# Kernel optimization log

Hardware: AMD Instinct MI355X
Metric: run time of the kernel (lower is better)

## Reference

```python
import jax, jax.numpy as jnp
import numpy as np

N_NODES = 20000
STEPS = 10  # message_passing_steps


def _mlp(x, p):
    # 3-layer MLP: Linear->ReLU->Linear->ReLU->Linear (no final activation)
    W1, b1, W2, b2, W3, b3 = p
    h = jax.nn.relu(x @ W1 + b1)
    h = jax.nn.relu(h @ W2 + b2)
    return h @ W3 + b3


def _aggregate(dst, edge_attr, num_nodes):
    # scatter_add of edge features into destination nodes, degree-normalized (deg clamped to >=1)
    agg = jax.ops.segment_sum(edge_attr, dst, num_segments=num_nodes)
    deg = jax.ops.segment_sum(jnp.ones((dst.shape[0], 1), edge_attr.dtype), dst, num_segments=num_nodes)
    return agg / jnp.maximum(deg, 1.0)


def setup_inputs() -> dict:
    key = jax.random.key(0)
    N, EM, EC = N_NODES, 120000, 20000
    ND, MD, CD, OD, L = 12, 7, 4, 3, 128
    keys = iter(jax.random.split(key, 128))

    def lin(i, o):
        return (jax.random.normal(next(keys), (i, o), jnp.float32) * 0.05,
                jax.random.normal(next(keys), (o,), jnp.float32) * 0.05)

    inp = {
        "node_x": jax.random.normal(next(keys), (N, ND), jnp.float32),
        "mesh_edge_attr": jax.random.normal(next(keys), (EM, MD), jnp.float32),
        "contact_edge_attr": jax.random.normal(next(keys), (EC, CD), jnp.float32),
    }
    dims = {"ne": (ND, L), "me": (MD, L), "ce": (CD, L), "pe": (3 * L, L), "pn": (3 * L, L), "de": (L, OD)}
    for name, (i, o) in dims.items():
        W1, b1 = lin(i, L)
        W2, b2 = lin(L, L)
        W3, b3 = lin(L, o)
        for pn, p in zip(["W1", "b1", "W2", "b2", "W3", "b3"], [W1, b1, W2, b2, W3, b3]):
            inp[name + "_" + pn] = p
    inp["mesh_edge_index"] = jax.random.randint(next(keys), (2, EM), 0, N)
    inp["contact_edge_index"] = jax.random.randint(next(keys), (2, EC), 0, N)
    return inp


def reference(node_x, mesh_edge_attr, contact_edge_attr,
              ne_W1, ne_b1, ne_W2, ne_b2, ne_W3, ne_b3,
              me_W1, me_b1, me_W2, me_b2, me_W3, me_b3,
              ce_W1, ce_b1, ce_W2, ce_b2, ce_W3, ce_b3,
              pe_W1, pe_b1, pe_W2, pe_b2, pe_W3, pe_b3,
              pn_W1, pn_b1, pn_W2, pn_b2, pn_W3, pn_b3,
              de_W1, de_b1, de_W2, de_b2, de_W3, de_b3,
              mesh_edge_index, contact_edge_index):
    ne = (ne_W1, ne_b1, ne_W2, ne_b2, ne_W3, ne_b3)
    mep = (me_W1, me_b1, me_W2, me_b2, me_W3, me_b3)
    cep = (ce_W1, ce_b1, ce_W2, ce_b2, ce_W3, ce_b3)
    pe = (pe_W1, pe_b1, pe_W2, pe_b2, pe_W3, pe_b3)
    pn = (pn_W1, pn_b1, pn_W2, pn_b2, pn_W3, pn_b3)
    de = (de_W1, de_b1, de_W2, de_b2, de_W3, de_b3)
    N = node_x.shape[0]
    # encode
    x = _mlp(node_x, ne)                 # [N, 128]
    me = _mlp(mesh_edge_attr, mep)       # [EM, 128]
    ce = _mlp(contact_edge_attr, cep)    # [EC, 128]
    msrc, mdst = mesh_edge_index[0], mesh_edge_index[1]
    csrc, cdst = contact_edge_index[0], contact_edge_index[1]
    # process (shared edge_mlp for both edge types, residual updates)
    for _ in range(STEPS):
        me = me + _mlp(jnp.concatenate([x[msrc], x[mdst], me], axis=-1), pe)
        ce = ce + _mlp(jnp.concatenate([x[csrc], x[cdst], ce], axis=-1), pe)
        agg_m = _aggregate(mdst, me, N)
        agg_c = _aggregate(cdst, ce, N)
        x = x + _mlp(jnp.concatenate([x, agg_m, agg_c], axis=-1), pn)
    # decode
    return _mlp(x, de)                   # [N, 3]
```

## Files before the change

### kernel.cpp

```cpp
#include <hip/hip_runtime.h>
#include <stdint.h>

typedef unsigned short u16;
typedef __attribute__((ext_vector_type(8))) short bf16x8;
typedef __attribute__((ext_vector_type(4))) float f32x4;

#define NNODES 20000
#define EM 120000
#define EC 20000
#define LDIM 128
#define MT 32
#define A_STR 392
#define H_STR 136

__device__ __forceinline__ u16 f2bf(float f){
  uint32_t b = __float_as_uint(f);
  b += 0x7FFF + ((b >> 16) & 1);
  return (u16)(b >> 16);
}

template<int KB>
__device__ __forceinline__ void layer(const u16* sIn, int in_str, const u16* Wp,
                                      int wr, int wc, int lane, f32x4 acc[4]){
  const int row = wr*16 + (lane & 15);
  const int kg  = lane >> 4;
  #pragma unroll
  for (int kb = 0; kb < KB; ++kb){
    bf16x8 a = *(const bf16x8*)(sIn + row*in_str + kb*32 + kg*8);
    const u16* wb = Wp + (((kb*8 + wc*4)*64 + lane) << 3);
    #pragma unroll
    for (int nf = 0; nf < 4; ++nf){
      bf16x8 b = *(const bf16x8*)(wb + (nf << 9));
      acc[nf] = __builtin_amdgcn_mfma_f32_16x16x32_bf16(a, b, acc[nf], 0, 0, 0);
    }
  }
}

__device__ __forceinline__ void hid_epi(f32x4 acc[4], const float* bias,
                                        int wr, int wc, int lane, u16* sOut){
  const int cl = lane & 15;
  const int r0 = wr*16 + (lane >> 4)*4;
  #pragma unroll
  for (int nf = 0; nf < 4; ++nf){
    int col = wc*64 + nf*16 + cl;
    float bv = bias[col];
    #pragma unroll
    for (int r = 0; r < 4; ++r){
      float v = acc[nf][r] + bv;
      sOut[(r0 + r)*H_STR + col] = f2bf(v > 0.f ? v : 0.f);
    }
  }
}

__device__ __forceinline__ void zero4(f32x4 acc[4]){
  const f32x4 vz = {0.f, 0.f, 0.f, 0.f};
  #pragma unroll
  for (int i = 0; i < 4; ++i) acc[i] = vz;
}

struct PackDesc { const float* src; int K_raw, N_raw, NF, elem_off; };
struct PackArgs { PackDesc d[18]; int total; };

__global__ __launch_bounds__(256) void pack_weights(PackArgs pa, u16* dst){
  int idx = blockIdx.x*256 + threadIdx.x;
  if (idx >= pa.total) return;
  int di = 0;
  #pragma unroll
  for (int i = 1; i < 18; ++i) if (idx >= pa.d[i].elem_off) di = i;
  PackDesc dd = pa.d[di];
  int e = idx - dd.elem_off;
  int f = e >> 9, lane = (e >> 3) & 63, j = e & 7;
  int kb = f / dd.NF, nf = f % dd.NF;
  int k = kb*32 + (lane >> 4)*8 + j;
  int n = nf*16 + (lane & 15);
  float v = (k < dd.K_raw && n < dd.N_raw) ? dd.src[k*dd.N_raw + n] : 0.f;
  dst[idx] = f2bf(v);
}

__global__ __launch_bounds__(256) void hist_kernel(const int* mdst, const int* cdst,
                                                   int* cnt_m, int* cnt_c){
  int i = blockIdx.x*256 + threadIdx.x;
  if (i < EM) atomicAdd(&cnt_m[mdst[i]], 1);
  else if (i < EM + EC) atomicAdd(&cnt_c[cdst[i - EM]], 1);
}

struct ScanArgs { const int *cnt_m, *cnt_c; int *start_m, *start_c, *cur_m, *cur_c; };

__global__ __launch_bounds__(256) void scan_kernel(ScanArgs a){
  const int n = NNODES;
  const int* cnt = blockIdx.x == 0 ? a.cnt_m : a.cnt_c;
  int* start     = blockIdx.x == 0 ? a.start_m : a.start_c;
  int* cur       = blockIdx.x == 0 ? a.cur_m : a.cur_c;
  __shared__ int part[256];
  __shared__ int base[257];
  int t = threadIdx.x;
  const int per = (n + 255) / 256;
  int lo = t*per, hi = min(n, lo + per);
  int s = 0;
  for (int j = lo; j < hi; ++j) s += cnt[j];
  part[t] = s;
  __syncthreads();
  if (t == 0){
    int run = 0;
    for (int i = 0; i < 256; ++i){ base[i] = run; run += part[i]; }
    base[256] = run;
  }
  __syncthreads();
  int run = base[t];
  for (int j = lo; j < hi; ++j){ start[j] = run; cur[j] = run; run += cnt[j]; }
  if (t == 255) start[n] = base[256];
}

__global__ __launch_bounds__(256) void scatter_kernel(const int* mdst, const int* cdst,
                                                      int* cur_m, int* cur_c,
                                                      int* eid_m, int* eid_c){
  int i = blockIdx.x*256 + threadIdx.x;
  if (i < EM){
    int p = atomicAdd(&cur_m[mdst[i]], 1);
    eid_m[p] = i;
  } else if (i < EM + EC){
    int e = i - EM;
    int p = atomicAdd(&cur_c[cdst[e]], 1);
    eid_c[p] = e;
  }
}

struct EncArgs {
  const float* in; int Kraw;
  const u16 *Wp1, *Wp2, *Wp3;
  const float *b1, *b2, *b3;
  float* out_f32; u16* out_b16;
};

__global__ __launch_bounds__(256) void enc_kernel(EncArgs a){
  __shared__ u16 sA[MT*A_STR];
  __shared__ u16 sH[MT*H_STR];
  const int tid = threadIdx.x, lane = tid & 63, w = tid >> 6, wr = w & 1, wc = w >> 1;
  const int m0 = blockIdx.x * MT;
  for (int i = tid; i < MT*32; i += 256){
    int row = i >> 5, c = i & 31;
    float v = (c < a.Kraw) ? a.in[(size_t)(m0 + row)*a.Kraw + c] : 0.f;
    sA[row*A_STR + c] = f2bf(v);
  }
  __syncthreads();
  f32x4 acc[4]; zero4(acc);
  layer<1>(sA, A_STR, a.Wp1, wr, wc, lane, acc);
  hid_epi(acc, a.b1, wr, wc, lane, sH);
  __syncthreads();
  zero4(acc);
  layer<4>(sH, H_STR, a.Wp2, wr, wc, lane, acc);
  hid_epi(acc, a.b2, wr, wc, lane, sA);
  __syncthreads();
  zero4(acc);
  layer<4>(sA, H_STR, a.Wp3, wr, wc, lane, acc);
  const int cl = lane & 15, r0l = wr*16 + (lane >> 4)*4;
  #pragma unroll
  for (int nf = 0; nf < 4; ++nf){
    int col = wc*64 + nf*16 + cl;
    float bv = a.b3[col];
    #pragma unroll
    for (int r = 0; r < 4; ++r){
      int m = m0 + r0l + r;
      float v = acc[nf][r] + bv;
      a.out_f32[(size_t)m*LDIM + col] = v;
      a.out_b16[(size_t)m*LDIM + col] = f2bf(v);
    }
  }
}

struct EdgeArgs {
  const u16 *Wp1, *Wp2, *Wp3;
  const float *b1, *b2, *b3;
  const u16* x_b16;
  const int *msrc, *mdst, *csrc, *cdst;
  u16 *me_b16, *ce_b16;
  float *me_f32, *ce_f32;
  int mesh_blocks;
};

__global__ __launch_bounds__(256) void edge_kernel(EdgeArgs a){
  __shared__ u16 sA[MT*A_STR];
  __shared__ u16 sH[MT*H_STR];
  const int tid = threadIdx.x, lane = tid & 63, w = tid >> 6, wr = w & 1, wc = w >> 1;
  const bool mesh = (int)blockIdx.x < a.mesh_blocks;
  const int e0 = (mesh ? (int)blockIdx.x : (int)blockIdx.x - a.mesh_blocks) * MT;
  const int* src = mesh ? a.msrc : a.csrc;
  const int* dst = mesh ? a.mdst : a.cdst;
  u16* fb   = mesh ? a.me_b16 : a.ce_b16;
  float* ff = mesh ? a.me_f32 : a.ce_f32;

  for (int i = tid; i < MT*48; i += 256){
    int row = i/48, ch = i%48;
    int e = e0 + row;
    const u16* sp;
    if (ch < 16)       sp = a.x_b16 + (size_t)src[e]*LDIM + ch*8;
    else if (ch < 32)  sp = a.x_b16 + (size_t)dst[e]*LDIM + (ch-16)*8;
    else               sp = fb + (size_t)e*LDIM + (ch-32)*8;
    *(bf16x8*)(sA + row*A_STR + ch*8) = *(const bf16x8*)sp;
  }
  __syncthreads();
  f32x4 acc[4]; zero4(acc);
  layer<12>(sA, A_STR, a.Wp1, wr, wc, lane, acc);
  hid_epi(acc, a.b1, wr, wc, lane, sH);
  __syncthreads();
  zero4(acc);
  layer<4>(sH, H_STR, a.Wp2, wr, wc, lane, acc);
  hid_epi(acc, a.b2, wr, wc, lane, sA);
  __syncthreads();
  zero4(acc);
  layer<4>(sA, H_STR, a.Wp3, wr, wc, lane, acc);

  const int cl = lane & 15, r0l = wr*16 + (lane >> 4)*4;
  #pragma unroll
  for (int r = 0; r < 4; ++r){
    int e = e0 + r0l + r;
    #pragma unroll
    for (int nf = 0; nf < 4; ++nf){
      int col = wc*64 + nf*16 + cl;
      float nv = ff[(size_t)e*LDIM + col] + acc[nf][r] + a.b3[col];
      ff[(size_t)e*LDIM + col] = nv;
      fb[(size_t)e*LDIM + col] = f2bf(nv);
    }
  }
}

struct NodeArgs {
  const u16 *Wp1, *Wp2, *Wp3;
  const float *b1, *b2, *b3;
  const u16* x_b16_in;
  const float *me_f32, *ce_f32;
  const int *start_m, *eid_m, *start_c, *eid_c;
  float* x_f32; u16* x_b16_out;
};

__global__ __launch_bounds__(256) void node_kernel(NodeArgs a){
  __shared__ u16 sA[MT*A_STR];
  __shared__ u16 sH[MT*H_STR];
  const int tid = threadIdx.x, lane = tid & 63, w = tid >> 6, wr = w & 1, wc = w >> 1;
  const int n0 = blockIdx.x * MT;

  for (int i = tid; i < MT*16; i += 256){
    int row = i >> 4, ch = i & 15;
    *(bf16x8*)(sA + row*A_STR + ch*8) = *(const bf16x8*)(a.x_b16_in + (size_t)(n0+row)*LDIM + ch*8);
  }

  {
    const int r = tid >> 3, c0 = (tid & 7) * 16;
    const int n = n0 + r;
    {
      int s = a.start_m[n], e = a.start_m[n+1];
      f32x4 a0{0,0,0,0}, a1{0,0,0,0}, a2{0,0,0,0}, a3{0,0,0,0};
      for (int j = s; j < e; ++j){
        const f32x4* p = (const f32x4*)(a.me_f32 + (size_t)a.eid_m[j]*LDIM + c0);
        a0 += p[0]; a1 += p[1]; a2 += p[2]; a3 += p[3];
      }
      float inv = 1.f / fmaxf((float)(e - s), 1.f);
      bf16x8 t0, t1;
      #pragma unroll
      for (int k = 0; k < 4; ++k){
        t0[k]   = (short)f2bf(a0[k]*inv); t0[k+4] = (short)f2bf(a1[k]*inv);
        t1[k]   = (short)f2bf(a2[k]*inv); t1[k+4] = (short)f2bf(a3[k]*inv);
      }
      *(bf16x8*)(sA + r*A_STR + 128 + c0) = t0;
      *(bf16x8*)(sA + r*A_STR + 128 + c0 + 8) = t1;
    }
    {
      int s = a.start_c[n], e = a.start_c[n+1];
      f32x4 a0{0,0,0,0}, a1{0,0,0,0}, a2{0,0,0,0}, a3{0,0,0,0};
      for (int j = s; j < e; ++j){
        const f32x4* p = (const f32x4*)(a.ce_f32 + (size_t)a.eid_c[j]*LDIM + c0);
        a0 += p[0]; a1 += p[1]; a2 += p[2]; a3 += p[3];
      }
      float inv = 1.f / fmaxf((float)(e - s), 1.f);
      bf16x8 t0, t1;
      #pragma unroll
      for (int k = 0; k < 4; ++k){
        t0[k]   = (short)f2bf(a0[k]*inv); t0[k+4] = (short)f2bf(a1[k]*inv);
        t1[k]   = (short)f2bf(a2[k]*inv); t1[k+4] = (short)f2bf(a3[k]*inv);
      }
      *(bf16x8*)(sA + r*A_STR + 256 + c0) = t0;
      *(bf16x8*)(sA + r*A_STR + 256 + c0 + 8) = t1;
    }
  }
  __syncthreads();
  f32x4 acc[4]; zero4(acc);
  layer<12>(sA, A_STR, a.Wp1, wr, wc, lane, acc);
  hid_epi(acc, a.b1, wr, wc, lane, sH);
  __syncthreads();
  zero4(acc);
  layer<4>(sH, H_STR, a.Wp2, wr, wc, lane, acc);
  hid_epi(acc, a.b2, wr, wc, lane, sA);
  __syncthreads();
  zero4(acc);
  layer<4>(sA, H_STR, a.Wp3, wr, wc, lane, acc);

  const int cl = lane & 15, r0l = wr*16 + (lane >> 4)*4;
  #pragma unroll
  for (int r = 0; r < 4; ++r){
    int n = n0 + r0l + r;
    #pragma unroll
    for (int nf = 0; nf < 4; ++nf){
      int col = wc*64 + nf*16 + cl;
      float nv = a.x_f32[(size_t)n*LDIM + col] + acc[nf][r] + a.b3[col];
      a.x_f32[(size_t)n*LDIM + col] = nv;
      a.x_b16_out[(size_t)n*LDIM + col] = f2bf(nv);
    }
  }
}

struct DecArgs {
  const u16 *Wp1, *Wp2, *Wp3;
  const float *b1, *b2, *b3;
  const u16* x_b16; float* out;
};

__global__ __launch_bounds__(256) void dec_kernel(DecArgs a){
  __shared__ u16 sA[MT*A_STR];
  __shared__ u16 sH[MT*H_STR];
  const int tid = threadIdx.x, lane = tid & 63, w = tid >> 6, wr = w & 1, wc = w >> 1;
  const int n0 = blockIdx.x * MT;
  for (int i = tid; i < MT*16; i += 256){
    int row = i >> 4, ch = i & 15;
    *(bf16x8*)(sA + row*H_STR + ch*8) = *(const bf16x8*)(a.x_b16 + (size_t)(n0+row)*LDIM + ch*8);
  }
  __syncthreads();
  f32x4 acc[4]; zero4(acc);
  layer<4>(sA, H_STR, a.Wp1, wr, wc, lane, acc);
  hid_epi(acc, a.b1, wr, wc, lane, sH);
  __syncthreads();
  zero4(acc);
  layer<4>(sH, H_STR, a.Wp2, wr, wc, lane, acc);
  hid_epi(acc, a.b2, wr, wc, lane, sA);
  __syncthreads();
  if (wc == 0){
    f32x4 a3 = {0.f, 0.f, 0.f, 0.f};
    const int row = wr*16 + (lane & 15), kg = lane >> 4;
    #pragma unroll
    for (int kb = 0; kb < 4; ++kb){
      bf16x8 av = *(const bf16x8*)(sA + row*H_STR + kb*32 + kg*8);
      bf16x8 bv = *(const bf16x8*)(a.Wp3 + ((kb*64 + lane) << 3));
      a3 = __builtin_amdgcn_mfma_f32_16x16x32_bf16(av, bv, a3, 0, 0, 0);
    }
    const int cl = lane & 15, r0l = wr*16 + (lane >> 4)*4;
    if (cl < 3){
      #pragma unroll
      for (int r = 0; r < 4; ++r)
        a.out[(size_t)(n0 + r0l + r)*3 + cl] = a3[r] + a.b3[cl];
    }
  }
}

extern "C" void kernel_launch(void* const* d_in, const int* in_sizes, int n_in,
                              void* d_out, int out_size, void* d_ws, size_t ws_size,
                              hipStream_t stream){
  auto F = [&](int i){ return (const float*)d_in[i]; };
  const float* node_x   = F(0);
  const float* mesh_attr = F(1);
  const float* cont_attr = F(2);
  const int* mei = (const int*)d_in[39];
  const int* cei = (const int*)d_in[40];
  const int *msrc = mei, *mdst = mei + EM, *csrc = cei, *cdst = cei + EC;

  char* ws = (char*)d_ws;
  size_t off = 0;
  auto take = [&](size_t b)->void*{ void* p = ws + off; off += (b + 255) & ~(size_t)255; return p; };
  float* x_f32  = (float*)take((size_t)NNODES*LDIM*4);
  u16*   x_b16  = (u16*)  take((size_t)NNODES*LDIM*2);
  float* me_f32 = (float*)take((size_t)EM*LDIM*4);
  u16*   me_b16 = (u16*)  take((size_t)EM*LDIM*2);
  float* ce_f32 = (float*)take((size_t)EC*LDIM*4);
  u16*   ce_b16 = (u16*)  take((size_t)EC*LDIM*2);
  u16*   wpack  = (u16*)  take((size_t)309248*2);
  int* cnt_m   = (int*)take((size_t)NNODES*4);
  int* cnt_c   = (int*)take((size_t)NNODES*4);
  int* start_m = (int*)take((size_t)(NNODES+1)*4);
  int* start_c = (int*)take((size_t)(NNODES+1)*4);
  int* cur_m   = (int*)take((size_t)NNODES*4);
  int* cur_c   = (int*)take((size_t)NNODES*4);
  int* eid_m   = (int*)take((size_t)EM*4);
  int* eid_c   = (int*)take((size_t)EC*4);

  static const int tbl[18][5] = {
    {3,12,128,32,128},{5,128,128,128,128},{7,128,128,128,128},
    {9,7,128,32,128},{11,128,128,128,128},{13,128,128,128,128},
    {15,4,128,32,128},{17,128,128,128,128},{19,128,128,128,128},
    {21,384,128,384,128},{23,128,128,128,128},{25,128,128,128,128},
    {27,384,128,384,128},{29,128,128,128,128},{31,128,128,128,128},
    {33,128,128,128,128},{35,128,128,128,128},{37,128,3,128,16}};
  PackArgs pa; int eo = 0; int offs[18];
  for (int i = 0; i < 18; ++i){
    offs[i] = eo;
    pa.d[i].src = F(tbl[i][0]);
    pa.d[i].K_raw = tbl[i][1];
    pa.d[i].N_raw = tbl[i][2];
    pa.d[i].NF = tbl[i][4] / 16;
    pa.d[i].elem_off = eo;
    eo += tbl[i][3] * tbl[i][4];
  }
  pa.total = eo;
  pack_weights<<<dim3(eo/256), dim3(256), 0, stream>>>(pa, wpack);

  size_t cnt_span = ((char*)cnt_c - (char*)cnt_m) + (size_t)NNODES*4;
  hipMemsetAsync(cnt_m, 0, cnt_span, stream);
  hist_kernel<<<dim3((EM + EC + 255)/256), dim3(256), 0, stream>>>(mdst, cdst, cnt_m, cnt_c);
  ScanArgs sa{cnt_m, cnt_c, start_m, start_c, cur_m, cur_c};
  scan_kernel<<<dim3(2), dim3(256), 0, stream>>>(sa);
  scatter_kernel<<<dim3((EM + EC + 255)/256), dim3(256), 0, stream>>>(mdst, cdst, cur_m, cur_c, eid_m, eid_c);

  EncArgs en{node_x, 12, wpack+offs[0], wpack+offs[1], wpack+offs[2], F(4), F(6), F(8), x_f32, x_b16};
  enc_kernel<<<dim3(NNODES/MT), dim3(256), 0, stream>>>(en);
  EncArgs em{mesh_attr, 7, wpack+offs[3], wpack+offs[4], wpack+offs[5], F(10), F(12), F(14), me_f32, me_b16};
  enc_kernel<<<dim3(EM/MT), dim3(256), 0, stream>>>(em);
  EncArgs ec{cont_attr, 4, wpack+offs[6], wpack+offs[7], wpack+offs[8], F(16), F(18), F(20), ce_f32, ce_b16};
  enc_kernel<<<dim3(EC/MT), dim3(256), 0, stream>>>(ec);

  EdgeArgs ea;
  ea.Wp1 = wpack+offs[9]; ea.Wp2 = wpack+offs[10]; ea.Wp3 = wpack+offs[11];
  ea.b1 = F(22); ea.b2 = F(24); ea.b3 = F(26);
  ea.x_b16 = x_b16;
  ea.msrc = msrc; ea.mdst = mdst; ea.csrc = csrc; ea.cdst = cdst;
  ea.me_b16 = me_b16; ea.ce_b16 = ce_b16;
  ea.me_f32 = me_f32; ea.ce_f32 = ce_f32;
  ea.mesh_blocks = EM/MT;

  NodeArgs na;
  na.Wp1 = wpack+offs[12]; na.Wp2 = wpack+offs[13]; na.Wp3 = wpack+offs[14];
  na.b1 = F(28); na.b2 = F(30); na.b3 = F(32);
  na.x_b16_in = x_b16;
  na.me_f32 = me_f32; na.ce_f32 = ce_f32;
  na.start_m = start_m; na.eid_m = eid_m; na.start_c = start_c; na.eid_c = eid_c;
  na.x_f32 = x_f32; na.x_b16_out = x_b16;

  for (int s = 0; s < 10; ++s){
    edge_kernel<<<dim3(EM/MT + EC/MT), dim3(256), 0, stream>>>(ea);
    node_kernel<<<dim3(NNODES/MT), dim3(256), 0, stream>>>(na);
  }

  DecArgs da{wpack+offs[15], wpack+offs[16], wpack+offs[17], F(34), F(36), F(38), x_b16, (float*)d_out};
  dec_kernel<<<dim3(NNODES/MT), dim3(256), 0, stream>>>(da);
}
```

Baseline: 1.428 ms.

## Enlarge edge/node MLP tiles to 64 rows with 8 waves and shared smem buffer

Edge and node kernels now process 64 rows per block with 512 threads (8 waves in a 2x4 grid), each wave computing a 32x32 output sub-tile as 2x2 MFMA fragments instead of 16x64. Each weight fragment load now feeds two MFMAs, and the hidden activations are written into the same shared buffer at a column offset, which drops the separate sH array. Tail handling clamps gather indices and guards the stores, since 20000/64 is not an integer. The larger block raises shared memory and register use per block and adds an extra barrier, which may lower occupancy.

```diff
diff --git a/kernel.cpp b/kernel.cpp
--- a/kernel.cpp
+++ b/kernel.cpp
@@ -10,6 +10,7 @@
 #define EC 20000
 #define LDIM 128
 #define MT 32
+#define MT2 64
 #define A_STR 392
 #define H_STR 136
 
@@ -56,6 +57,53 @@
   const f32x4 vz = {0.f, 0.f, 0.f, 0.f};
   #pragma unroll
   for (int i = 0; i < 4; ++i) acc[i] = vz;
+}
+
+template<int KB>
+__device__ __forceinline__ void layer64(const u16* sIn, const u16* Wp,
+                                        int wr, int wc, int lane, f32x4 acc[2][2]){
+  const int r0 = wr*32 + (lane & 15);
+  const int kg = lane >> 4;
+  const u16* a0p = sIn + r0*A_STR + kg*8;
+  const u16* a1p = a0p + 16*A_STR;
+  const u16* wb  = Wp + (((wc*2)*64 + lane) << 3);
+  #pragma unroll
+  for (int kb = 0; kb < KB; ++kb){
+    bf16x8 a0 = *(const bf16x8*)(a0p + kb*32);
+    bf16x8 a1 = *(const bf16x8*)(a1p + kb*32);
+    const u16* wk = wb + kb*4096;
+    bf16x8 b0 = *(const bf16x8*)(wk);
+    bf16x8 b1 = *(const bf16x8*)(wk + 512);
+    acc[0][0] = __builtin_amdgcn_mfma_f32_16x16x32_bf16(a0, b0, acc[0][0], 0, 0, 0);
+    acc[1][0] = __builtin_amdgcn_mfma_f32_16x16x32_bf16(a1, b0, acc[1][0], 0, 0, 0);
+    acc[0][1] = __builtin_amdgcn_mfma_f32_16x16x32_bf16(a0, b1, acc[0][1], 0, 0, 0);
+    acc[1][1] = __builtin_amdgcn_mfma_f32_16x16x32_bf16(a1, b1, acc[1][1], 0, 0, 0);
+  }
+}
+
+__device__ __forceinline__ void hid_epi64(f32x4 acc[2][2], const float* bias,
+                                          int wr, int wc, int lane, u16* sOut){
+  const int cl = lane & 15;
+  const int rq = (lane >> 4)*4;
+  #pragma unroll
+  for (int rf = 0; rf < 2; ++rf){
+    int r0 = wr*32 + rf*16 + rq;
+    #pragma unroll
+    for (int nf = 0; nf < 2; ++nf){
+      int col = wc*32 + nf*16 + cl;
+      float bv = bias[col];
+      #pragma unroll
+      for (int r = 0; r < 4; ++r){
+        float v = acc[rf][nf][r] + bv;
+        sOut[(r0 + r)*A_STR + col] = f2bf(v > 0.f ? v : 0.f);
+      }
+    }
+  }
+}
+
+__device__ __forceinline__ void zero22(f32x4 acc[2][2]){
+  const f32x4 vz = {0.f, 0.f, 0.f, 0.f};
+  acc[0][0] = vz; acc[0][1] = vz; acc[1][0] = vz; acc[1][1] = vz;
 }
 
 struct PackDesc { const float* src; int K_raw, N_raw, NF, elem_off; };
@@ -178,20 +226,20 @@
   int mesh_blocks;
 };
 
-__global__ __launch_bounds__(256) void edge_kernel(EdgeArgs a){
-  __shared__ u16 sA[MT*A_STR];
-  __shared__ u16 sH[MT*H_STR];
+__global__ __launch_bounds__(512) void edge_kernel(EdgeArgs a){
+  __shared__ u16 sA[MT2*A_STR];
   const int tid = threadIdx.x, lane = tid & 63, w = tid >> 6, wr = w & 1, wc = w >> 1;
   const bool mesh = (int)blockIdx.x < a.mesh_blocks;
-  const int e0 = (mesh ? (int)blockIdx.x : (int)blockIdx.x - a.mesh_blocks) * MT;
+  const int e0 = (mesh ? (int)blockIdx.x : (int)blockIdx.x - a.mesh_blocks) * MT2;
+  const int E = mesh ? EM : EC;
   const int* src = mesh ? a.msrc : a.csrc;
   const int* dst = mesh ? a.mdst : a.cdst;
   u16* fb   = mesh ? a.me_b16 : a.ce_b16;
   float* ff = mesh ? a.me_f32 : a.ce_f32;
 
-  for (int i = tid; i < MT*48; i += 256){
+  for (int i = tid; i < MT2*48; i += 512){
     int row = i/48, ch = i%48;
-    int e = e0 + row;
+    int e = e0 + row; if (e >= E) e = E - 1;
     const u16* sp;
     if (ch < 16)       sp = a.x_b16 + (size_t)src[e]*LDIM + ch*8;
     else if (ch < 32)  sp = a.x_b16 + (size_t)dst[e]*LDIM + (ch-16)*8;
@@ -199,27 +247,33 @@
     *(bf16x8*)(sA + row*A_STR + ch*8) = *(const bf16x8*)sp;
   }
   __syncthreads();
-  f32x4 acc[4]; zero4(acc);
-  layer<12>(sA, A_STR, a.Wp1, wr, wc, lane, acc);
-  hid_epi(acc, a.b1, wr, wc, lane, sH);
-  __syncthreads();
-  zero4(acc);
-  layer<4>(sH, H_STR, a.Wp2, wr, wc, lane, acc);
-  hid_epi(acc, a.b2, wr, wc, lane, sA);
-  __syncthreads();
-  zero4(acc);
-  layer<4>(sA, H_STR, a.Wp3, wr, wc, lane, acc);
-
-  const int cl = lane & 15, r0l = wr*16 + (lane >> 4)*4;
-  #pragma unroll
-  for (int r = 0; r < 4; ++r){
-    int e = e0 + r0l + r;
-    #pragma unroll
-    for (int nf = 0; nf < 4; ++nf){
-      int col = wc*64 + nf*16 + cl;
-      float nv = ff[(size_t)e*LDIM + col] + acc[nf][r] + a.b3[col];
-      ff[(size_t)e*LDIM + col] = nv;
-      fb[(size_t)e*LDIM + col] = f2bf(nv);
+  f32x4 acc[2][2]; zero22(acc);
+  layer64<12>(sA, a.Wp1, wr, wc, lane, acc);
+  __syncthreads();
+  hid_epi64(acc, a.b1, wr, wc, lane, sA + 256);
+  __syncthreads();
+  zero22(acc);
+  layer64<4>(sA + 256, a.Wp2, wr, wc, lane, acc);
+  hid_epi64(acc, a.b2, wr, wc, lane, sA);
+  __syncthreads();
+  zero22(acc);
+  layer64<4>(sA, a.Wp3, wr, wc, lane, acc);
+
+  const int cl = lane & 15, rq = (lane >> 4)*4;
+  #pragma unroll
+  for (int rf = 0; rf < 2; ++rf){
+    #pragma unroll
+    for (int r = 0; r < 4; ++r){
+      int e = e0 + wr*32 + rf*16 + rq + r;
+      if (e < E){
+        #pragma unroll
+        for (int nf = 0; nf < 2; ++nf){
+          int col = wc*32 + nf*16 + cl;
+          float nv = ff[(size_t)e*LDIM + col] + acc[rf][nf][r] + a.b3[col];
+          ff[(size_t)e*LDIM + col] = nv;
+          fb[(size_t)e*LDIM + col] = f2bf(nv);
+        }
+      }
     }
   }
 }
@@ -233,22 +287,23 @@
   float* x_f32; u16* x_b16_out;
 };
 
-__global__ __launch_bounds__(256) void node_kernel(NodeArgs a){
-  __shared__ u16 sA[MT*A_STR];
-  __shared__ u16 sH[MT*H_STR];
+__global__ __launch_bounds__(512) void node_kernel(NodeArgs a){
+  __shared__ u16 sA[MT2*A_STR];
   const int tid = threadIdx.x, lane = tid & 63, w = tid >> 6, wr = w & 1, wc = w >> 1;
-  const int n0 = blockIdx.x * MT;
-
-  for (int i = tid; i < MT*16; i += 256){
+  const int n0 = blockIdx.x * MT2;
+
+  for (int i = tid; i < MT2*16; i += 512){
     int row = i >> 4, ch = i & 15;
-    *(bf16x8*)(sA + row*A_STR + ch*8) = *(const bf16x8*)(a.x_b16_in + (size_t)(n0+row)*LDIM + ch*8);
+    int n = n0 + row; if (n >= NNODES) n = NNODES - 1;
+    *(bf16x8*)(sA + row*A_STR + ch*8) = *(const bf16x8*)(a.x_b16_in + (size_t)n*LDIM + ch*8);
   }
 
   {
     const int r = tid >> 3, c0 = (tid & 7) * 16;
     const int n = n0 + r;
+    const bool ok = n < NNODES;
     {
-      int s = a.start_m[n], e = a.start_m[n+1];
+      int s = ok ? a.start_m[n] : 0, e = ok ? a.start_m[n+1] : 0;
       f32x4 a0{0,0,0,0}, a1{0,0,0,0}, a2{0,0,0,0}, a3{0,0,0,0};
       for (int j = s; j < e; ++j){
         const f32x4* p = (const f32x4*)(a.me_f32 + (size_t)a.eid_m[j]*LDIM + c0);
@@ -265,7 +320,7 @@
       *(bf16x8*)(sA + r*A_STR + 128 + c0 + 8) = t1;
     }
     {
-      int s = a.start_c[n], e = a.start_c[n+1];
+      int s = ok ? a.start_c[n] : 0, e = ok ? a.start_c[n+1] : 0;
       f32x4 a0{0,0,0,0}, a1{0,0,0,0}, a2{0,0,0,0}, a3{0,0,0,0};
       for (int j = s; j < e; ++j){
         const f32x4* p = (const f32x4*)(a.ce_f32 + (size_t)a.eid_c[j]*LDIM + c0);
@@ -283,27 +338,33 @@
     }
   }
   __syncthreads();
-  f32x4 acc[4]; zero4(acc);
-  layer<12>(sA, A_STR, a.Wp1, wr, wc, lane, acc);
-  hid_epi(acc, a.b1, wr, wc, lane, sH);
-  __syncthreads();
-  zero4(acc);
-  layer<4>(sH, H_STR, a.Wp2, wr, wc, lane, acc);
-  hid_epi(acc, a.b2, wr, wc, lane, sA);
-  __syncthreads();
-  zero4(acc);
-  layer<4>(sA, H_STR, a.Wp3, wr, wc, lane, acc);
-
-  const int cl = lane & 15, r0l = wr*16 + (lane >> 4)*4;
-  #pragma unroll
-  for (int r = 0; r < 4; ++r){
-    int n = n0 + r0l + r;
-    #pragma unroll
-    for (int nf = 0; nf < 4; ++nf){
-      int col = wc*64 + nf*16 + cl;
-      float nv = a.x_f32[(size_t)n*LDIM + col] + acc[nf][r] + a.b3[col];
-      a.x_f32[(size_t)n*LDIM + col] = nv;
-      a.x_b16_out[(size_t)n*LDIM + col] = f2bf(nv);
+  f32x4 acc[2][2]; zero22(acc);
+  layer64<12>(sA, a.Wp1, wr, wc, lane, acc);
+  __syncthreads();
+  hid_epi64(acc, a.b1, wr, wc, lane, sA + 256);
+  __syncthreads();
+  zero22(acc);
+  layer64<4>(sA + 256, a.Wp2, wr, wc, lane, acc);
+  hid_epi64(acc, a.b2, wr, wc, lane, sA);
+  __syncthreads();
+  zero22(acc);
+  layer64<4>(sA, a.Wp3, wr, wc, lane, acc);
+
+  const int cl = lane & 15, rq = (lane >> 4)*4;
+  #pragma unroll
+  for (int rf = 0; rf < 2; ++rf){
+    #pragma unroll
+    for (int r = 0; r < 4; ++r){
+      int n = n0 + wr*32 + rf*16 + rq + r;
+      if (n < NNODES){
+        #pragma unroll
+        for (int nf = 0; nf < 2; ++nf){
+          int col = wc*32 + nf*16 + cl;
+          float nv = a.x_f32[(size_t)n*LDIM + col] + acc[rf][nf][r] + a.b3[col];
+          a.x_f32[(size_t)n*LDIM + col] = nv;
+          a.x_b16_out[(size_t)n*LDIM + col] = f2bf(nv);
+        }
+      }
     }
   }
 }
@@ -421,7 +482,7 @@
   ea.msrc = msrc; ea.mdst = mdst; ea.csrc = csrc; ea.cdst = cdst;
   ea.me_b16 = me_b16; ea.ce_b16 = ce_b16;
   ea.me_f32 = me_f32; ea.ce_f32 = ce_f32;
-  ea.mesh_blocks = EM/MT;
+  ea.mesh_blocks = EM/MT2;
 
   NodeArgs na;
   na.Wp1 = wpack+offs[12]; na.Wp2 = wpack+offs[13]; na.Wp3 = wpack+offs[14];
@@ -431,9 +492,11 @@
   na.start_m = start_m; na.eid_m = eid_m; na.start_c = start_c; na.eid_c = eid_c;
   na.x_f32 = x_f32; na.x_b16_out = x_b16;
 
+  const int edge_blocks = EM/MT2 + (EC + MT2 - 1)/MT2;
+  const int node_blocks = (NNODES + MT2 - 1)/MT2;
   for (int s = 0; s < 10; ++s){
-    edge_kernel<<<dim3(EM/MT + EC/MT), dim3(256), 0, stream>>>(ea);
-    node_kernel<<<dim3(NNODES/MT), dim3(256), 0, stream>>>(na);
+    edge_kernel<<<dim3(edge_blocks), dim3(512), 0, stream>>>(ea);
+    node_kernel<<<dim3(node_blocks), dim3(512), 0, stream>>>(na);
   }
 
   DecArgs da{wpack+offs[15], wpack+offs[16], wpack+offs[17], F(34), F(36), F(38), x_b16, (float*)d_out};
```

Result: faster. 1.230 ms (-13.8%).
